# Kernel optimization log

Measured on AMD Instinct MI355X. Metric: run time of the kernel, lower is better.

The kernel has to match this reference:

```python
import jax, jax.numpy as jnp
import numpy as np

B, S, D = 8, 1024, 512
H = W = 32          # S = H * W, square 2D layout
N, K = 16, 32       # num_heads, head_size


def _reindexed_bias(rel_bias):
    # rel_bias: [N, 2H-1, 2W-1] -> [N, S, S]
    # bias[n, s, t] = rel_bias[n, h_s - h_t + H - 1, w_s - w_t + W - 1]
    pos = jnp.arange(S)
    hh = pos // W
    ww = pos % W
    dh = hh[:, None] - hh[None, :] + (H - 1)  # [S, S] in [0, 2H-2]
    dw = ww[:, None] - ww[None, :] + (W - 1)  # [S, S] in [0, 2W-2]
    return rel_bias[:, dh, dw]  # [N, S, S]


def setup_inputs() -> dict:
    key = jax.random.key(0)
    ks = jax.random.split(key, 10)
    std = 0.02
    query = jax.random.normal(ks[0], (B, S, D), dtype=jnp.float32)
    Wq = jax.random.normal(ks[1], (D, N, K), dtype=jnp.float32) * std
    bq = jnp.zeros((N, K), dtype=jnp.float32)
    Wk = jax.random.normal(ks[2], (D, N, K), dtype=jnp.float32) * std
    bk = jnp.zeros((N, K), dtype=jnp.float32)
    Wv = jax.random.normal(ks[3], (D, N, K), dtype=jnp.float32) * std
    bv = jnp.zeros((N, K), dtype=jnp.float32)
    Wo = jax.random.normal(ks[4], (N, K, D), dtype=jnp.float32) * std
    bo = jnp.zeros((D,), dtype=jnp.float32)
    rel_bias = jax.random.normal(ks[5], (N, 2 * H - 1, 2 * W - 1), dtype=jnp.float32) * std
    return {"query": query, "Wq": Wq, "bq": bq, "Wk": Wk, "bk": bk,
            "Wv": Wv, "bv": bv, "Wo": Wo, "bo": bo, "rel_bias": rel_bias}


def reference(query, Wq, bq, Wk, bk, Wv, bv, Wo, bo, rel_bias):
    q_scale = K ** (-0.5)
    # TrailDense projections: BSD,DNK->BSNK (+ bias)
    q = jnp.einsum('bsd,dnk->bsnk', query, Wq) + bq
    k = jnp.einsum('btd,dnk->btnk', query, Wk) + bk
    v = jnp.einsum('btd,dnk->btnk', query, Wv) + bv
    q = q * q_scale
    logits = jnp.einsum('bsnk,btnk->bnst', q, k)
    logits = logits + _reindexed_bias(rel_bias)[None]  # broadcast over batch
    # float32 softmax, cast back to input dtype
    probs = jax.nn.softmax(logits.astype(jnp.float32), axis=-1).astype(logits.dtype)
    attn_out = jnp.einsum('bnst,btnk->bsnk', probs, v)
    # output projection: BSNK,NKD->BSD (+ bias)
    out = jnp.einsum('bsnk,nkd->bsd', attn_out, Wo) + bo
    return out
```

## Files before the change

### kernel.cpp

```cpp
#include <hip/hip_runtime.h>
#include <stdint.h>


typedef unsigned short u16;
typedef unsigned int   u32;
typedef float  f32x4  __attribute__((ext_vector_type(4)));
typedef float  f32x16 __attribute__((ext_vector_type(16)));
typedef __bf16 bf16x8 __attribute__((ext_vector_type(8)));

#define DEV static __device__ __forceinline__

DEV u16 f2bf(float f){ union { float f; u32 u; } c; c.f = f; u32 x = c.u;
                       return (u16)((x + 0x7fffu + ((x >> 16) & 1u)) >> 16); }
DEV bf16x8 as_bf8(uint4 v){ return __builtin_bit_cast(bf16x8, v); }

__global__ __launch_bounds__(256) void k_wtrans(
    const float* __restrict__ Wq, const float* __restrict__ Wk,
    const float* __restrict__ Wv, const float* __restrict__ Wo,
    u16* __restrict__ WT)
{
  __shared__ float tile[64][65];
  const float* src = (blockIdx.z == 0) ? Wq : (blockIdx.z == 1) ? Wk
                   : (blockIdx.z == 2) ? Wv : Wo;
  u16* dst = WT + blockIdx.z * 512 * 512;
  const int t = threadIdx.x;
  const int r0 = blockIdx.y * 64, c0 = blockIdx.x * 64;
  #pragma unroll
  for (int p = 0; p < 4; p++){
    int r = p * 16 + (t >> 4), c = (t & 15) * 4;
    float4 v = *(const float4*)&src[(r0 + r) * 512 + c0 + c];
    tile[r][c+0] = v.x; tile[r][c+1] = v.y; tile[r][c+2] = v.z; tile[r][c+3] = v.w;
  }
  __syncthreads();
  #pragma unroll
  for (int p = 0; p < 2; p++){
    int rr = p * 32 + (t >> 3), cc = (t & 7) * 8;
    u32 d[4];
    #pragma unroll
    for (int j = 0; j < 4; j++){
      u32 lo = f2bf(tile[cc + 2*j][rr]);
      u32 hh = f2bf(tile[cc + 2*j + 1][rr]);
      d[j] = lo | (hh << 16);
    }
    uint4 v; v.x = d[0]; v.y = d[1]; v.z = d[2]; v.w = d[3];
    *(uint4*)&dst[(c0 + rr) * 512 + r0 + cc] = v;
  }
}

__global__ __launch_bounds__(256) void k_qkv(
    const float* __restrict__ X, const u16* __restrict__ WT,
    const float* __restrict__ bq, const float* __restrict__ bk, const float* __restrict__ bv,
    u16* __restrict__ Qo, u16* __restrict__ Ko, u16* __restrict__ Vt)
{
  __shared__ u16 sm[2][128][72];
  const int mode = blockIdx.z;
  const u16* W = WT + mode * (512 * 512);
  const int m0 = blockIdx.x * 128, n0 = blockIdx.y * 128;
  const int t = threadIdx.x, lane = t & 63, w = t >> 6;
  const int wr = w >> 1, wc = w & 1, lr = lane & 15, hi = lane >> 4;
  f32x4 acc[4][4] = {};
  for (int d0 = 0; d0 < 512; d0 += 64){
    #pragma unroll
    for (int p = 0; p < 8; p++){
      int r = p * 16 + (t >> 4), c4 = (t & 15) * 4;
      float4 v = *(const float4*)&X[(m0 + r) * 512 + d0 + c4];
      uint2 pk2;
      pk2.x = (u32)f2bf(v.x) | ((u32)f2bf(v.y) << 16);
      pk2.y = (u32)f2bf(v.z) | ((u32)f2bf(v.w) << 16);
      *(uint2*)&sm[0][r][c4] = pk2;
    }
    #pragma unroll
    for (int p = 0; p < 4; p++){
      int r = p * 32 + (t >> 3), ch = (t & 7) * 8;
      *(uint4*)&sm[1][r][ch] = *(const uint4*)&W[(n0 + r) * 512 + d0 + ch];
    }
    __syncthreads();
    #pragma unroll
    for (int kc = 0; kc < 2; kc++){
      bf16x8 a[4], b[4];
      #pragma unroll
      for (int i = 0; i < 4; i++){
        a[i] = as_bf8(*(const uint4*)&sm[0][wr*64 + i*16 + lr][kc*32 + hi*8]);
        b[i] = as_bf8(*(const uint4*)&sm[1][wc*64 + i*16 + lr][kc*32 + hi*8]);
      }
      #pragma unroll
      for (int i = 0; i < 4; i++)
        #pragma unroll
        for (int j = 0; j < 4; j++)
          acc[i][j] = __builtin_amdgcn_mfma_f32_16x16x32_bf16(a[i], b[j], acc[i][j], 0, 0, 0);
    }
    __syncthreads();
  }
  const float* bias = (mode == 0) ? bq : (mode == 1) ? bk : bv;
  float bv4[4];
  #pragma unroll
  for (int j = 0; j < 4; j++) bv4[j] = bias[n0 + wc*64 + j*16 + lr];

  if (mode < 2){
    u16* Out = (mode == 0) ? Qo : Ko;
    const float scale = (mode == 0) ? 0.17677669529663687f : 1.0f;
    u16* ep = &sm[0][0][0] + w * 4608;
    #pragma unroll
    for (int i = 0; i < 4; i++)
      #pragma unroll
      for (int j = 0; j < 4; j++)
        #pragma unroll
        for (int r = 0; r < 4; r++){
          float v = (acc[i][j][r] + bv4[j]) * scale;
          ep[(i*16 + hi*4 + r) * 72 + j*16 + lr] = f2bf(v);
        }
    __syncthreads();
    #pragma unroll
    for (int p = 0; p < 8; p++){
      int rr = p * 8 + (lane >> 3), cc = (lane & 7) * 8;
      uint4 v = *(uint4*)&ep[rr * 72 + cc];
      int gm = m0 + wr*64 + rr;
      int gc = n0 + wc*64 + cc;
      int b = gm >> 10, s = gm & 1023, n = gc >> 5, kk = gc & 31;
      *(uint4*)&Out[((b*16 + n)*1024 + s)*32 + kk] = v;
    }
  } else {
    #pragma unroll
    for (int i = 0; i < 4; i++)
      #pragma unroll
      for (int j = 0; j < 4; j++){
        int gm = m0 + wr*64 + i*16 + hi*4;
        int gc = n0 + wc*64 + j*16 + lr;
        int b = gm >> 10, s = gm & 1023, n = gc >> 5, kk = gc & 31;
        u32 d0 = (u32)f2bf(acc[i][j][0] + bv4[j]) | ((u32)f2bf(acc[i][j][1] + bv4[j]) << 16);
        u32 d1 = (u32)f2bf(acc[i][j][2] + bv4[j]) | ((u32)f2bf(acc[i][j][3] + bv4[j]) << 16);
        uint2 vv; vv.x = d0; vv.y = d1;
        *(uint2*)&Vt[(((b*16 + n)*32 + kk) * 1024) + s] = vv;
      }
  }
}

__global__ __launch_bounds__(256) void k_attn(
    const u16* __restrict__ Q, const u16* __restrict__ Kg,
    const u16* __restrict__ Vt, const float* __restrict__ relb,
    u16* __restrict__ AO)
{
  __shared__ float bias_s[63 * 63];
  __shared__ u16 ks[64][40];
  __shared__ u16 vs[32][72];
  const int t = threadIdx.x, lane = t & 63, w = t >> 6;
  const int hi = lane >> 5, lq = lane & 31;
  const int bid = blockIdx.x;
  const int qt = bid & 7, bn = bid >> 3, n = bn & 15;
  const int q0 = qt * 128 + w * 32;
  const u16* Qp = Q  + (bn * 1024 + q0) * 32;
  const u16* Kp = Kg + bn * 1024 * 32;
  const u16* Vp = Vt + bn * 32 * 1024;
  const float* rb = relb + n * 63 * 63;
  for (int i = t; i < 63 * 63; i += 256) bias_s[i] = rb[i];

  bf16x8 qf[2];
  #pragma unroll
  for (int kc = 0; kc < 2; kc++)
    qf[kc] = as_bf8(*(const uint4*)&Qp[lq*32 + kc*16 + hi*8]);
  const int h_q = q0 >> 5;

  f32x16 oacc = {};
  float mrun = -1.0e30f, lsum = 0.f;

  for (int t0 = 0; t0 < 1024; t0 += 64){
    {
      int r = t >> 2, ch = (t & 3) * 8;
      *(uint4*)&ks[r][ch] = *(const uint4*)&Kp[(t0 + r) * 32 + ch];
      int r2 = t >> 3, c2 = (t & 7) * 8;
      *(uint4*)&vs[r2][c2] = *(const uint4*)&Vp[r2 * 1024 + t0 + c2];
    }
    __syncthreads();

    float p[32];
    float tmax = -1.0e30f;
    #pragma unroll
    for (int ts = 0; ts < 2; ts++){
      f32x16 c = {};
      bf16x8 kf0 = as_bf8(*(const uint4*)&ks[ts*32 + lq][hi*8]);
      bf16x8 kf1 = as_bf8(*(const uint4*)&ks[ts*32 + lq][16 + hi*8]);
      c = __builtin_amdgcn_mfma_f32_32x32x16_bf16(kf0, qf[0], c, 0, 0, 0);
      c = __builtin_amdgcn_mfma_f32_32x32x16_bf16(kf1, qf[1], c, 0, 0, 0);
      const int dh = h_q - (t0 >> 5) - ts + 31;
      const int bbase = dh * 63 + 31 + lq - hi * 4;
      #pragma unroll
      for (int r = 0; r < 16; r++){
        int tl = (r & 3) + 8 * (r >> 2);
        float v = c[r] + bias_s[bbase - tl];
        p[ts*16 + r] = v;
        tmax = fmaxf(tmax, v);
      }
    }
    tmax = fmaxf(tmax, __shfl_xor(tmax, 32));
    float mn = fmaxf(mrun, tmax);
    float alpha = __expf(mrun - mn);
    mrun = mn;
    lsum *= alpha;
    #pragma unroll
    for (int r = 0; r < 16; r++) oacc[r] *= alpha;
    #pragma unroll
    for (int i = 0; i < 32; i++){ p[i] = __expf(p[i] - mn); lsum += p[i]; }

    u32 pk[16], ot[16];
    #pragma unroll
    for (int e = 0; e < 16; e++)
      pk[e] = (u32)f2bf(p[2*e]) | ((u32)f2bf(p[2*e + 1]) << 16);
    #pragma unroll
    for (int e = 0; e < 16; e++)
      ot[e] = (u32)__shfl_xor((int)pk[e], 32);

    #pragma unroll
    for (int tc = 0; tc < 4; tc++){
      int base = (tc >> 1) * 8 + (tc & 1) * 4;
      uint4 bb;
      if (hi == 0){ bb.x = pk[base];   bb.y = pk[base+1]; bb.z = ot[base];   bb.w = ot[base+1]; }
      else        { bb.x = ot[base+2]; bb.y = ot[base+3]; bb.z = pk[base+2]; bb.w = pk[base+3]; }
      bf16x8 pb = as_bf8(bb);
      bf16x8 vf = as_bf8(*(const uint4*)&vs[lq][tc*16 + hi*8]);
      oacc = __builtin_amdgcn_mfma_f32_32x32x16_bf16(vf, pb, oacc, 0, 0, 0);
    }
    __syncthreads();
  }
  lsum += __shfl_xor(lsum, 32);
  float inv = 1.0f / lsum;
  const int b = bn >> 4;
  u16* op = AO + ((b * 1024 + q0 + lq) * 16 + n) * 32;
  #pragma unroll
  for (int g = 0; g < 4; g++){
    u32 d0 = (u32)f2bf(oacc[g*4+0] * inv) | ((u32)f2bf(oacc[g*4+1] * inv) << 16);
    u32 d1 = (u32)f2bf(oacc[g*4+2] * inv) | ((u32)f2bf(oacc[g*4+3] * inv) << 16);
    uint2 vv; vv.x = d0; vv.y = d1;
    *(uint2*)&op[g*8 + hi*4] = vv;
  }
}

__global__ __launch_bounds__(256) void k_out(
    const u16* __restrict__ Ain, const u16* __restrict__ WoT,
    const float* __restrict__ bo, float* __restrict__ Out)
{
  __shared__ u16 sm[2][128][72];
  const int m0 = blockIdx.x * 128, n0 = blockIdx.y * 128;
  const int t = threadIdx.x, lane = t & 63, w = t >> 6;
  const int wr = w >> 1, wc = w & 1, lr = lane & 15, hi = lane >> 4;
  f32x4 acc[4][4] = {};
  for (int d0 = 0; d0 < 512; d0 += 64){
    #pragma unroll
    for (int p = 0; p < 4; p++){
      int r = p * 32 + (t >> 3), ch = (t & 7) * 8;
      *(uint4*)&sm[0][r][ch] = *(const uint4*)&Ain[(m0 + r) * 512 + d0 + ch];
      *(uint4*)&sm[1][r][ch] = *(const uint4*)&WoT[(n0 + r) * 512 + d0 + ch];
    }
    __syncthreads();
    #pragma unroll
    for (int kc = 0; kc < 2; kc++){
      bf16x8 a[4], b[4];
      #pragma unroll
      for (int i = 0; i < 4; i++){
        a[i] = as_bf8(*(const uint4*)&sm[0][wr*64 + i*16 + lr][kc*32 + hi*8]);
        b[i] = as_bf8(*(const uint4*)&sm[1][wc*64 + i*16 + lr][kc*32 + hi*8]);
      }
      #pragma unroll
      for (int i = 0; i < 4; i++)
        #pragma unroll
        for (int j = 0; j < 4; j++)
          acc[i][j] = __builtin_amdgcn_mfma_f32_16x16x32_bf16(a[i], b[j], acc[i][j], 0, 0, 0);
    }
    __syncthreads();
  }
  float bv4[4];
  #pragma unroll
  for (int j = 0; j < 4; j++) bv4[j] = bo[n0 + wc*64 + j*16 + lr];
  #pragma unroll
  for (int i = 0; i < 4; i++)
    #pragma unroll
    for (int j = 0; j < 4; j++)
      #pragma unroll
      for (int r = 0; r < 4; r++)
        Out[(m0 + wr*64 + i*16 + hi*4 + r) * 512 + n0 + wc*64 + j*16 + lr]
            = acc[i][j][r] + bv4[j];
}

extern "C" void kernel_launch(void* const* d_in, const int* in_sizes, int n_in,
                              void* d_out, int out_size, void* d_ws, size_t ws_size,
                              hipStream_t stream)
{
  const float* query = (const float*)d_in[0];
  const float* Wq    = (const float*)d_in[1];
  const float* bq    = (const float*)d_in[2];
  const float* Wk    = (const float*)d_in[3];
  const float* bk    = (const float*)d_in[4];
  const float* Wv    = (const float*)d_in[5];
  const float* bv    = (const float*)d_in[6];
  const float* Wo    = (const float*)d_in[7];
  const float* bo    = (const float*)d_in[8];
  const float* relb  = (const float*)d_in[9];
  float* out = (float*)d_out;

  u16* WT  = (u16*)d_ws;
  u16* Qw  = WT  + 4 * 512 * 512;
  u16* Kw  = Qw  + 8 * 16 * 1024 * 32;
  u16* Vtw = Kw  + 8 * 16 * 1024 * 32;
  u16* Aw  = Vtw + 8 * 16 * 1024 * 32;

  k_wtrans<<<dim3(8, 8, 4), dim3(256), 0, stream>>>(Wq, Wk, Wv, Wo, WT);
  k_qkv  <<<dim3(64, 4, 3), dim3(256), 0, stream>>>(query, WT, bq, bk, bv, Qw, Kw, Vtw);
  k_attn <<<dim3(1024),     dim3(256), 0, stream>>>(Qw, Kw, Vtw, relb, Aw);
  k_out  <<<dim3(64, 4),    dim3(256), 0, stream>>>(Aw, WT + 3 * 512 * 512, bo, out);
}
```

Before: 116.8 us.

## Drop online-softmax max tracking, use exp2 with fixed offset and hardware bf16 pack

```diff
diff --git a/kernel.cpp b/kernel.cpp
--- a/kernel.cpp
+++ b/kernel.cpp
@@ -10,9 +10,24 @@
 
 #define DEV static __device__ __forceinline__
 
+#if __has_builtin(__builtin_amdgcn_exp2f)
+#define EXP2(x) __builtin_amdgcn_exp2f(x)
+#else
+#define EXP2(x) exp2f(x)
+#endif
+
 DEV u16 f2bf(float f){ union { float f; u32 u; } c; c.f = f; u32 x = c.u;
                        return (u16)((x + 0x7fffu + ((x >> 16) & 1u)) >> 16); }
+DEV u32 cvtpk(float lo, float hh){
+  u32 r; asm("v_cvt_pk_bf16_f32 %0, %1, %2" : "=v"(r) : "v"(lo), "v"(hh));
+  return r;
+}
+DEV void plswap(u32 &a, u32 &b){
+  asm("v_permlane32_swap_b32 %0, %1" : "+v"(a), "+v"(b));
+}
 DEV bf16x8 as_bf8(uint4 v){ return __builtin_bit_cast(bf16x8, v); }
+
+#define LOG2E 1.4426950408889634f
 
 __global__ __launch_bounds__(256) void k_wtrans(
     const float* __restrict__ Wq, const float* __restrict__ Wk,
@@ -35,14 +50,11 @@
   #pragma unroll
   for (int p = 0; p < 2; p++){
     int rr = p * 32 + (t >> 3), cc = (t & 7) * 8;
-    u32 d[4];
-    #pragma unroll
-    for (int j = 0; j < 4; j++){
-      u32 lo = f2bf(tile[cc + 2*j][rr]);
-      u32 hh = f2bf(tile[cc + 2*j + 1][rr]);
-      d[j] = lo | (hh << 16);
-    }
-    uint4 v; v.x = d[0]; v.y = d[1]; v.z = d[2]; v.w = d[3];
+    uint4 v;
+    v.x = cvtpk(tile[cc+0][rr], tile[cc+1][rr]);
+    v.y = cvtpk(tile[cc+2][rr], tile[cc+3][rr]);
+    v.z = cvtpk(tile[cc+4][rr], tile[cc+5][rr]);
+    v.w = cvtpk(tile[cc+6][rr], tile[cc+7][rr]);
     *(uint4*)&dst[(c0 + rr) * 512 + r0 + cc] = v;
   }
 }
@@ -64,9 +76,7 @@
     for (int p = 0; p < 8; p++){
       int r = p * 16 + (t >> 4), c4 = (t & 15) * 4;
       float4 v = *(const float4*)&X[(m0 + r) * 512 + d0 + c4];
-      uint2 pk2;
-      pk2.x = (u32)f2bf(v.x) | ((u32)f2bf(v.y) << 16);
-      pk2.y = (u32)f2bf(v.z) | ((u32)f2bf(v.w) << 16);
+      uint2 pk2; pk2.x = cvtpk(v.x, v.y); pk2.y = cvtpk(v.z, v.w);
       *(uint2*)&sm[0][r][c4] = pk2;
     }
     #pragma unroll
@@ -98,7 +108,7 @@
 
   if (mode < 2){
     u16* Out = (mode == 0) ? Qo : Ko;
-    const float scale = (mode == 0) ? 0.17677669529663687f : 1.0f;
+    const float scale = (mode == 0) ? (0.17677669529663687f * LOG2E) : 1.0f;
     u16* ep = &sm[0][0][0] + w * 4608;
     #pragma unroll
     for (int i = 0; i < 4; i++)
@@ -127,9 +137,9 @@
         int gm = m0 + wr*64 + i*16 + hi*4;
         int gc = n0 + wc*64 + j*16 + lr;
         int b = gm >> 10, s = gm & 1023, n = gc >> 5, kk = gc & 31;
-        u32 d0 = (u32)f2bf(acc[i][j][0] + bv4[j]) | ((u32)f2bf(acc[i][j][1] + bv4[j]) << 16);
-        u32 d1 = (u32)f2bf(acc[i][j][2] + bv4[j]) | ((u32)f2bf(acc[i][j][3] + bv4[j]) << 16);
-        uint2 vv; vv.x = d0; vv.y = d1;
+        uint2 vv;
+        vv.x = cvtpk(acc[i][j][0] + bv4[j], acc[i][j][1] + bv4[j]);
+        vv.y = cvtpk(acc[i][j][2] + bv4[j], acc[i][j][3] + bv4[j]);
         *(uint2*)&Vt[(((b*16 + n)*32 + kk) * 1024) + s] = vv;
       }
   }
@@ -141,96 +151,76 @@
     u16* __restrict__ AO)
 {
   __shared__ float bias_s[63 * 63];
-  __shared__ u16 ks[64][40];
-  __shared__ u16 vs[32][72];
   const int t = threadIdx.x, lane = t & 63, w = t >> 6;
   const int hi = lane >> 5, lq = lane & 31;
-  const int bid = blockIdx.x;
+  const int bid = ((blockIdx.x & 7) << 7) | (blockIdx.x >> 3);
   const int qt = bid & 7, bn = bid >> 3, n = bn & 15;
   const int q0 = qt * 128 + w * 32;
   const u16* Qp = Q  + (bn * 1024 + q0) * 32;
   const u16* Kp = Kg + bn * 1024 * 32;
   const u16* Vp = Vt + bn * 32 * 1024;
   const float* rb = relb + n * 63 * 63;
-  for (int i = t; i < 63 * 63; i += 256) bias_s[i] = rb[i];
+  for (int i = t; i < 63 * 63; i += 256) bias_s[i] = rb[i] * LOG2E - 8.0f;
 
   bf16x8 qf[2];
   #pragma unroll
   for (int kc = 0; kc < 2; kc++)
     qf[kc] = as_bf8(*(const uint4*)&Qp[lq*32 + kc*16 + hi*8]);
   const int h_q = q0 >> 5;
+  __syncthreads();
 
   f32x16 oacc = {};
-  float mrun = -1.0e30f, lsum = 0.f;
+  float ls0 = 0.f, ls1 = 0.f;
 
   for (int t0 = 0; t0 < 1024; t0 += 64){
-    {
-      int r = t >> 2, ch = (t & 3) * 8;
-      *(uint4*)&ks[r][ch] = *(const uint4*)&Kp[(t0 + r) * 32 + ch];
-      int r2 = t >> 3, c2 = (t & 7) * 8;
-      *(uint4*)&vs[r2][c2] = *(const uint4*)&Vp[r2 * 1024 + t0 + c2];
-    }
-    __syncthreads();
-
-    float p[32];
-    float tmax = -1.0e30f;
+    uint4 kv[4], vv[4];
+    #pragma unroll
+    for (int ts = 0; ts < 2; ts++){
+      kv[ts*2+0] = *(const uint4*)&Kp[(t0 + ts*32 + lq)*32 + hi*8];
+      kv[ts*2+1] = *(const uint4*)&Kp[(t0 + ts*32 + lq)*32 + 16 + hi*8];
+    }
+    #pragma unroll
+    for (int tc = 0; tc < 4; tc++)
+      vv[tc] = *(const uint4*)&Vp[lq*1024 + t0 + tc*16 + hi*8];
+
+    u32 pk[16];
     #pragma unroll
     for (int ts = 0; ts < 2; ts++){
       f32x16 c = {};
-      bf16x8 kf0 = as_bf8(*(const uint4*)&ks[ts*32 + lq][hi*8]);
-      bf16x8 kf1 = as_bf8(*(const uint4*)&ks[ts*32 + lq][16 + hi*8]);
-      c = __builtin_amdgcn_mfma_f32_32x32x16_bf16(kf0, qf[0], c, 0, 0, 0);
-      c = __builtin_amdgcn_mfma_f32_32x32x16_bf16(kf1, qf[1], c, 0, 0, 0);
+      c = __builtin_amdgcn_mfma_f32_32x32x16_bf16(as_bf8(kv[ts*2+0]), qf[0], c, 0, 0, 0);
+      c = __builtin_amdgcn_mfma_f32_32x32x16_bf16(as_bf8(kv[ts*2+1]), qf[1], c, 0, 0, 0);
       const int dh = h_q - (t0 >> 5) - ts + 31;
       const int bbase = dh * 63 + 31 + lq - hi * 4;
       #pragma unroll
-      for (int r = 0; r < 16; r++){
+      for (int r = 0; r < 16; r += 2){
         int tl = (r & 3) + 8 * (r >> 2);
-        float v = c[r] + bias_s[bbase - tl];
-        p[ts*16 + r] = v;
-        tmax = fmaxf(tmax, v);
-      }
-    }
-    tmax = fmaxf(tmax, __shfl_xor(tmax, 32));
-    float mn = fmaxf(mrun, tmax);
-    float alpha = __expf(mrun - mn);
-    mrun = mn;
-    lsum *= alpha;
-    #pragma unroll
-    for (int r = 0; r < 16; r++) oacc[r] *= alpha;
-    #pragma unroll
-    for (int i = 0; i < 32; i++){ p[i] = __expf(p[i] - mn); lsum += p[i]; }
-
-    u32 pk[16], ot[16];
-    #pragma unroll
-    for (int e = 0; e < 16; e++)
-      pk[e] = (u32)f2bf(p[2*e]) | ((u32)f2bf(p[2*e + 1]) << 16);
-    #pragma unroll
-    for (int e = 0; e < 16; e++)
-      ot[e] = (u32)__shfl_xor((int)pk[e], 32);
-
+        float v0 = EXP2(c[r]   + bias_s[bbase - tl]);
+        float v1 = EXP2(c[r+1] + bias_s[bbase - tl - 1]);
+        ls0 += v0; ls1 += v1;
+        pk[ts*8 + (r >> 1)] = cvtpk(v0, v1);
+      }
+    }
     #pragma unroll
     for (int tc = 0; tc < 4; tc++){
-      int base = (tc >> 1) * 8 + (tc & 1) * 4;
-      uint4 bb;
-      if (hi == 0){ bb.x = pk[base];   bb.y = pk[base+1]; bb.z = ot[base];   bb.w = ot[base+1]; }
-      else        { bb.x = ot[base+2]; bb.y = ot[base+3]; bb.z = pk[base+2]; bb.w = pk[base+3]; }
-      bf16x8 pb = as_bf8(bb);
-      bf16x8 vf = as_bf8(*(const uint4*)&vs[lq][tc*16 + hi*8]);
-      oacc = __builtin_amdgcn_mfma_f32_32x32x16_bf16(vf, pb, oacc, 0, 0, 0);
-    }
-    __syncthreads();
-  }
+      u32 a0 = pk[tc*4+0], b0 = pk[tc*4+2];
+      u32 a1 = pk[tc*4+1], b1 = pk[tc*4+3];
+      plswap(a0, b0);
+      plswap(a1, b1);
+      uint4 bb; bb.x = a0; bb.y = a1; bb.z = b0; bb.w = b1;
+      oacc = __builtin_amdgcn_mfma_f32_32x32x16_bf16(as_bf8(vv[tc]), as_bf8(bb), oacc, 0, 0, 0);
+    }
+  }
+  float lsum = ls0 + ls1;
   lsum += __shfl_xor(lsum, 32);
   float inv = 1.0f / lsum;
   const int b = bn >> 4;
   u16* op = AO + ((b * 1024 + q0 + lq) * 16 + n) * 32;
   #pragma unroll
   for (int g = 0; g < 4; g++){
-    u32 d0 = (u32)f2bf(oacc[g*4+0] * inv) | ((u32)f2bf(oacc[g*4+1] * inv) << 16);
-    u32 d1 = (u32)f2bf(oacc[g*4+2] * inv) | ((u32)f2bf(oacc[g*4+3] * inv) << 16);
-    uint2 vv; vv.x = d0; vv.y = d1;
-    *(uint2*)&op[g*8 + hi*4] = vv;
+    uint2 vv2;
+    vv2.x = cvtpk(oacc[g*4+0] * inv, oacc[g*4+1] * inv);
+    vv2.y = cvtpk(oacc[g*4+2] * inv, oacc[g*4+3] * inv);
+    *(uint2*)&op[g*8 + hi*4] = vv2;
   }
 }
 
```

After: 95.84 us. -17.9%, faster.
